# Optimization experiments

Hardware: AMD Instinct MI355X
Metric: run time of the kernel (lower is better)

The kernel has to match this reference:

```python
import jax, jax.numpy as jnp
import numpy as np

B, NV, FD = 16, 128, 8192
T_TEMP = 0.2      # self.T
MARGIN = 1.0      # nn.TripletMarginLoss default
EPS = 1e-6        # pairwise_distance eps


def _l2norm(x):
    # torch F.normalize(dim=1): x / max(||x||, 1e-12)
    nrm = jnp.maximum(jnp.linalg.norm(x, axis=-1, keepdims=True), 1e-12)
    return x / nrm


def _ssl_parts(qb, kb, nb, num_gt):
    # qb,kb,nb: [NV, FD] flattened reid embeddings for one image
    qv = _l2norm(qb)[:num_gt]          # [g, FD]
    kv = _l2norm(kb)[:num_gt]          # [g, FD]
    nv = _l2norm(nb)                   # [NV, FD] (negatives are NOT sliced)
    g = num_gt
    S = qv @ kv.T                      # [g, g] all pairwise dots (replaces torch.dot loops)
    # similarity-matrix loss
    sm = jnp.sum((S - jnp.eye(g, dtype=S.dtype)) ** 2) / (g * g)
    # pairwise distances with torch eps convention: ||a - b + eps||_2
    # = sqrt(||a||^2 + ||b||^2 - 2 a.b + 2*eps*(sum(a)-sum(b)) + D*eps^2); ||a||=||b||=1
    sq = qv.sum(axis=1)                # [g]
    sk = kv.sum(axis=1)                # [g]
    const = FD * EPS * EPS
    d_qk = jnp.sqrt(jnp.maximum(2.0 - 2.0 * S + 2.0 * EPS * (sq[:, None] - sk[None, :]) + const, 0.0))
    d_kq = jnp.sqrt(jnp.maximum(2.0 - 2.0 * S.T + 2.0 * EPS * (sk[:, None] - sq[None, :]) + const, 0.0))
    off = 1.0 - jnp.eye(g, dtype=S.dtype)
    # triplet: anc=q_i,pos=k_i,neg=k_j  and  anc=k_i,pos=q_i,neg=q_j, j != i
    tri1 = jnp.sum(jax.nn.relu(jnp.diag(d_qk)[:, None] - d_qk + MARGIN) * off)
    tri2 = jnp.sum(jax.nn.relu(jnp.diag(d_kq)[:, None] - d_kq + MARGIN) * off)
    tri_sum = tri1 + tri2
    # cycle consistency: |q_i.k_j - k_i.q_j| = |S[i,j] - S[j,i]|
    cyc = jnp.sum(jnp.abs(S - S.T) * off) / (g * (g - 1))
    # InfoNCE: l_pos = q_i.k_i, l_neg = q @ n.T
    l_pos = jnp.diag(S)[:, None]       # [g, 1]
    l_neg = qv @ nv.T                  # [g, NV]
    logits = jnp.concatenate([l_pos, l_neg], axis=1) / T_TEMP
    ce = jnp.mean(jax.nn.logsumexp(logits, axis=1) - logits[:, 0])  # CE with labels=0
    return sm, tri_sum, cyc, ce / g


def setup_inputs() -> dict:
    key = jax.random.key(0)
    kq, kk, kn = jax.random.split(key, 3)
    q = jax.random.normal(kq, (B, NV, FD), dtype=jnp.float32)
    k = jax.random.normal(kk, (B, NV, FD), dtype=jnp.float32)
    n = jax.random.normal(kn, (B, NV, FD), dtype=jnp.float32)
    return {"q": q, "k": k, "n": n, "num_gt": NV}


def reference(q, k, n, num_gt):
    sm, tri, cyc, ce = jax.vmap(lambda a, b, c: _ssl_parts(a, b, c, num_gt))(q, k, n)
    tri_cnt = 2 * num_gt * (num_gt - 1)
    # original bug: tri_loss accumulates across batches while tri_cnt resets,
    # so each batch contributes cumsum(tri)[b] / tri_cnt
    ssl = jnp.sum(sm) + jnp.sum(jnp.cumsum(tri)) / tri_cnt + jnp.sum(cyc) + jnp.sum(ce)
    return ssl
```

## Files before the change

kernel.cpp:

```cpp
#include <hip/hip_runtime.h>
#include <cstdint>
#include <cstddef>

#define B_N   16
#define G_N   128
#define FD_N  8192
#define KSPLIT 16
#define KC    512
#define BK2   32
#define NITER 16

typedef unsigned short u16;
typedef u16  u16x8 __attribute__((ext_vector_type(8)));
typedef __bf16 bf16x8 __attribute__((ext_vector_type(8)));
typedef float f32x16 __attribute__((ext_vector_type(16)));

#define QSUM_P   0
#define QSSQ_P   32768
#define KSUM_P   65536
#define KSSQ_P   98304
#define NSSQ_P   131072
#define SM_ROW   163840
#define CE_ROW   165888
#define S_OFF    167936
#define PART_OFF_F 430080

__device__ __forceinline__ u16 f2bf(float f) {
    uint32_t u = __float_as_uint(f);
    u += 0x7FFFu + ((u >> 16) & 1u);
    return (u16)(u >> 16);
}

__device__ __forceinline__ void load_lds16(const float* g, float* l) {
    __builtin_amdgcn_global_load_lds(
        (__attribute__((address_space(1))) void*)(g),
        (__attribute__((address_space(3))) void*)(l),
        16, 0, 0);
}

#define WAITV4() asm volatile("s_waitcnt vmcnt(4)" ::: "memory")
#define WAITV0() asm volatile("s_waitcnt vmcnt(0)" ::: "memory")

__global__ __launch_bounds__(512, 4)
void k_gemm(const float* __restrict__ q, const float* __restrict__ kM,
            const float* __restrict__ nM, float* __restrict__ ws)
{
    __shared__ __align__(16) float sA[2][G_N * BK2];
    __shared__ __align__(16) float sB[2][G_N * BK2];

    const int tid = threadIdx.x;
    const int blk = blockIdx.x;
    const int b    = blk >> 5;
    const int rem  = blk & 31;
    const int half = rem >> 4;
    const int kch  = rem & 15;

    const int lane  = tid & 63;
    const int wv    = tid >> 6;
    const int wm    = wv >> 2;
    const int wn    = wv & 3;
    const int khalf = lane >> 5;
    const int lrow  = lane & 31;
    const int rA0 = wm*64 + lrow;
    const int rB0 = wn*32 + lrow;
    const bool statA = (wn == 0);
    const bool statB = (wm == 0);

    const size_t mat_off = (size_t)b * (G_N * FD_N) + (size_t)kch * KC;
    const float* Ap = q + mat_off;
    const float* Bp = (half ? nM : kM) + mat_off;

    const int r0s = wv*16 + (lane >> 3);
    const int r1s = r0s + 8;
    const size_t goff0 = (size_t)r0s * FD_N + (size_t)(((lane & 7) ^ (r0s & 7)) << 2);
    const size_t goff1 = (size_t)r1s * FD_N + (size_t)(((lane & 7) ^ (r1s & 7)) << 2);
    const int lds0 = wv * 512;
    const int lds1 = wv * 512 + 256;

#define STAGE(ST, T) do {                                                     \
        const size_t tof_ = (size_t)((T) * BK2);                              \
        load_lds16(Ap + goff0 + tof_, &sA[ST][lds0]);                         \
        load_lds16(Bp + goff0 + tof_, &sB[ST][lds0]);                         \
        load_lds16(Ap + goff1 + tof_, &sA[ST][lds1]);                         \
        load_lds16(Bp + goff1 + tof_, &sB[ST][lds1]);                         \
    } while (0)

#define LOADCVT(SP, R, CH, FR, EN, SS, QQ) do {                               \
        const int x_ = (R) & 7;                                               \
        const float* rp_ = (SP) + (R) * BK2;                                  \
        float4 lo_ = *(const float4*)(rp_ + ((((CH)*2    ) ^ x_) << 2));      \
        float4 hi_ = *(const float4*)(rp_ + ((((CH)*2 + 1) ^ x_) << 2));      \
        if (EN) {                                                             \
            SS += (lo_.x + lo_.y) + (lo_.z + lo_.w)                           \
                + (hi_.x + hi_.y) + (hi_.z + hi_.w);                          \
            QQ += lo_.x*lo_.x + lo_.y*lo_.y + lo_.z*lo_.z + lo_.w*lo_.w       \
                + hi_.x*hi_.x + hi_.y*hi_.y + hi_.z*hi_.z + hi_.w*hi_.w;      \
        }                                                                     \
        u16x8 h_;                                                             \
        h_[0]=f2bf(lo_.x); h_[1]=f2bf(lo_.y); h_[2]=f2bf(lo_.z); h_[3]=f2bf(lo_.w); \
        h_[4]=f2bf(hi_.x); h_[5]=f2bf(hi_.y); h_[6]=f2bf(hi_.z); h_[7]=f2bf(hi_.w); \
        FR = __builtin_bit_cast(bf16x8, h_);                                  \
    } while (0)

#define COMPUTE_PHASE(ST) do {                                                \
        const float* sAp_ = &sA[ST][0];                                       \
        const float* sBp_ = &sB[ST][0];                                       \
        _Pragma("unroll")                                                     \
        for (int s = 0; s < 2; ++s) {                                         \
            const int ch = s*2 + khalf;                                       \
            bf16x8 af0, af1, bfv;                                             \
            LOADCVT(sAp_, rA0,      ch, af0, statA, aS0, aQ0);                \
            LOADCVT(sAp_, rA0 + 32, ch, af1, statA, aS1, aQ1);                \
            LOADCVT(sBp_, rB0,      ch, bfv, statB, bS0, bQ0);                \
            acc[0] = __builtin_amdgcn_mfma_f32_32x32x16_bf16(af0, bfv, acc[0], 0, 0, 0); \
            acc[1] = __builtin_amdgcn_mfma_f32_32x32x16_bf16(af1, bfv, acc[1], 0, 0, 0); \
        }                                                                     \
    } while (0)

    float aS0 = 0.f, aQ0 = 0.f, aS1 = 0.f, aQ1 = 0.f, bS0 = 0.f, bQ0 = 0.f;

    f32x16 acc[2];
    #pragma unroll
    for (int mb = 0; mb < 2; ++mb)
      #pragma unroll
      for (int e = 0; e < 16; ++e) acc[mb][e] = 0.f;

    STAGE(0, 0);
    STAGE(1, 1);

    for (int t = 0; t < 14; t += 2) {
        WAITV4();
        __builtin_amdgcn_s_barrier();
        COMPUTE_PHASE(0);
        __builtin_amdgcn_s_barrier();
        STAGE(0, t + 2);

        WAITV4();
        __builtin_amdgcn_s_barrier();
        COMPUTE_PHASE(1);
        __builtin_amdgcn_s_barrier();
        STAGE(1, t + 3);
    }
    WAITV4();
    __builtin_amdgcn_s_barrier();
    COMPUTE_PHASE(0);
    __builtin_amdgcn_s_barrier();
    WAITV0();
    __builtin_amdgcn_s_barrier();
    COMPUTE_PHASE(1);

    u16* part = (u16*)(ws + PART_OFF_F) + ((size_t)blk << 14);
    #pragma unroll
    for (int mb = 0; mb < 2; ++mb) {
        int col = wn*32 + lrow;
        int rbase = wm*64 + mb*32 + 4*khalf;
        #pragma unroll
        for (int reg = 0; reg < 16; ++reg) {
            int row = rbase + (reg & 3) + 8*(reg >> 2);
            part[row*G_N + col] = f2bf(acc[mb][reg]);
        }
    }

    if (statA) {
        aS0 += __shfl_xor(aS0, 32, 64); aQ0 += __shfl_xor(aQ0, 32, 64);
        aS1 += __shfl_xor(aS1, 32, 64); aQ1 += __shfl_xor(aQ1, 32, 64);
        if (half == 0 && khalf == 0) {
            int o = kch*2048 + b*G_N + wm*64 + lrow;
            ws[QSUM_P + o]      = aS0; ws[QSSQ_P + o]      = aQ0;
            ws[QSUM_P + o + 32] = aS1; ws[QSSQ_P + o + 32] = aQ1;
        }
    }
    if (statB) {
        bS0 += __shfl_xor(bS0, 32, 64); bQ0 += __shfl_xor(bQ0, 32, 64);
        if (khalf == 0) {
            int o = kch*2048 + b*G_N + wn*32 + lrow;
            if (half == 0) { ws[KSUM_P + o] = bS0; ws[KSSQ_P + o] = bQ0; }
            else           { ws[NSSQ_P + o] = bQ0; }
        }
    }
#undef STAGE
#undef LOADCVT
#undef COMPUTE_PHASE
}

__global__ __launch_bounds__(256)
void k_red2(float* __restrict__ ws, float* __restrict__ out)
{
    const int blk  = blockIdx.x;
    const int b    = blk >> 4;
    const int half = (blk >> 3) & 1;
    const int rg   = blk & 7;
    const int t    = threadIdx.x;
    const int lr   = t >> 4;
    const int i    = rg*16 + lr;
    const int c8   = t & 15;
    __shared__ float nrm[128];
    __shared__ float invq_s[16];

    if (blk == 0 && t == 0) out[0] = 0.f;

    if (t < 128) {
        float ss = 0.f;
        const float* p = ws + (half ? NSSQ_P : KSSQ_P) + b*G_N + t;
        #pragma unroll
        for (int kc2 = 0; kc2 < KSPLIT; ++kc2) ss += p[kc2*2048];
        nrm[t] = 1.f / fmaxf(sqrtf(ss), 1e-12f);
    } else if (t < 144) {
        float ss = 0.f;
        const float* p = ws + QSSQ_P + b*G_N + rg*16 + (t - 128);
        #pragma unroll
        for (int kc2 = 0; kc2 < KSPLIT; ++kc2) ss += p[kc2*2048];
        invq_s[t-128] = 1.f / fmaxf(sqrtf(ss), 1e-12f);
    }
    __syncthreads();

    const u16* part = (const u16*)(ws + PART_OFF_F);
    float s[8] = {0,0,0,0,0,0,0,0};
    #pragma unroll
    for (int kc2 = 0; kc2 < KSPLIT; ++kc2) {
        size_t idx = ((size_t)(b*32 + half*16 + kc2) << 14) + i*G_N + c8*8;
        u16x8 h = *(const u16x8*)(part + idx);
        #pragma unroll
        for (int e = 0; e < 8; ++e)
            s[e] += __uint_as_float(((uint32_t)h[e]) << 16);
    }
    const float iq = invq_s[lr];
    if (half == 0) {
        float smacc = 0.f;
        float S8[8];
        #pragma unroll
        for (int e = 0; e < 8; ++e) {
            int j = c8*8 + e;
            S8[e] = s[e] * iq * nrm[j];
            float d = S8[e] - (j == i ? 1.f : 0.f);
            smacc += d*d;
        }
        float* Sp = ws + S_OFF + (size_t)b*16384 + i*G_N + c8*8;
        float4 w0 = {S8[0],S8[1],S8[2],S8[3]};
        float4 w1 = {S8[4],S8[5],S8[6],S8[7]};
        *(float4*)Sp = w0; *(float4*)(Sp+4) = w1;
        #pragma unroll
        for (int m = 8; m >= 1; m >>= 1) smacc += __shfl_xor(smacc, m, 64);
        if (c8 == 0) ws[SM_ROW + b*G_N + i] = smacc;
    } else {
        float eacc = 0.f;
        #pragma unroll
        for (int e = 0; e < 8; ++e)
            eacc += __expf(5.f * s[e] * iq * nrm[c8*8+e]);
        #pragma unroll
        for (int m = 8; m >= 1; m >>= 1) eacc += __shfl_xor(eacc, m, 64);
        if (c8 == 0) ws[CE_ROW + b*G_N + i] = eacc;
    }
}

__global__ __launch_bounds__(256)
void k_epi(float* __restrict__ ws, float* __restrict__ out)
{
    const int blk = blockIdx.x;
    const int b   = blk >> 3;
    const int i0  = (blk & 7) * 16;
    const int t   = threadIdx.x;
    __shared__ float sqv[128], skv[128], ddq[128], ddk[128];
    __shared__ float rbuf[4];
    const float c0 = (float)FD_N * 1e-6f * 1e-6f;

    const float* S = ws + S_OFF + (size_t)b * 16384;
    if (t < 128) {
        float qs=0, qq=0, ks=0, kq=0;
        #pragma unroll
        for (int kc2 = 0; kc2 < KSPLIT; ++kc2) {
            int o = kc2*2048 + b*G_N + t;
            qs += ws[QSUM_P + o]; qq += ws[QSSQ_P + o];
            ks += ws[KSUM_P + o]; kq += ws[KSSQ_P + o];
        }
        float iq = 1.f/fmaxf(sqrtf(qq),1e-12f);
        float ik = 1.f/fmaxf(sqrtf(kq),1e-12f);
        float sq = qs*iq, sk = ks*ik;
        sqv[t]=sq; skv[t]=sk;
        float Stt = S[t*G_N + t];
        ddq[t] = sqrtf(fmaxf(2.f - 2.f*Stt + 2e-6f*(sq-sk) + c0, 0.f));
        ddk[t] = sqrtf(fmaxf(2.f - 2.f*Stt + 2e-6f*(sk-sq) + c0, 0.f));
    }
    __syncthreads();

    float tri=0.f, cyc=0.f, ce=0.f, sm=0.f;
    #pragma unroll
    for (int p = 0; p < 8; ++p) {
        int idx = p*256 + t;
        int i = i0 + (idx >> 7), j = idx & 127;
        if (i != j) {
            float S_ij = S[i*G_N + j];
            float dqk = sqrtf(fmaxf(2.f - 2.f*S_ij + 2e-6f*(sqv[i]-skv[j]) + c0, 0.f));
            tri += fmaxf(ddq[i] - dqk + 1.f, 0.f);
            float dkq = sqrtf(fmaxf(2.f - 2.f*S_ij + 2e-6f*(skv[j]-sqv[i]) + c0, 0.f));
            tri += fmaxf(ddk[j] - dkq + 1.f, 0.f);
            cyc += fabsf(S_ij - S[j*G_N + i]);
        }
    }
    if (t < 16) {
        int r = i0 + t;
        float lp = 5.f * S[r*G_N + r];
        ce = __logf(ws[CE_ROW + b*G_N + r] + __expf(lp)) - lp;
        sm = ws[SM_ROW + b*G_N + r];
    }
    float contrib = sm * (1.f/16384.f) + cyc * (1.f/16256.f) + ce * (1.f/16384.f)
                  + (float)(B_N - b) * tri * (1.f/32512.f);
    #pragma unroll
    for (int m = 32; m >= 1; m >>= 1) contrib += __shfl_xor(contrib, m, 64);
    if ((t & 63) == 0) rbuf[t >> 6] = contrib;
    __syncthreads();
    if (t == 0) atomicAdd(out, rbuf[0] + rbuf[1] + rbuf[2] + rbuf[3]);
}

extern "C" void kernel_launch(void* const* d_in, const int* in_sizes, int n_in,
                              void* d_out, int out_size, void* d_ws, size_t ws_size,
                              hipStream_t stream)
{
    const float* q  = (const float*)d_in[0];
    const float* kM = (const float*)d_in[1];
    const float* nM = (const float*)d_in[2];
    float* ws  = (float*)d_ws;
    float* out = (float*)d_out;

    k_gemm<<<B_N * 2 * KSPLIT, 512, 0, stream>>>(q, kM, nM, ws);
    k_red2<<<256, 256, 0, stream>>>(ws, out);
    k_epi<<<128, 256, 0, stream>>>(ws, out);
}
```

Baseline: 219.6 us.

## Restructure GEMM to stage q rows in LDS as bf16 and stream k/n from global

Each block now converts a 32-row by 2048-wide slice of q to bf16 once and keeps it in LDS (about 128 KB). Eight waves then stream k or n rows directly from global memory into MFMA operands, with no LDS double-buffering for B. The K split drops from 16 to 4 chunks, which shrinks the partial-sum buffer, changes its layout, and makes the reduction kernels cheaper. In exchange, k and n are re-read once per row group (four times in total, possibly absorbed by L2), only one block fits per CU, and global load latency is hidden only by loop unrolling.

```diff
diff --git a/kernel.cpp b/kernel.cpp
--- a/kernel.cpp
+++ b/kernel.cpp
@@ -5,10 +5,9 @@
 #define B_N   16
 #define G_N   128
 #define FD_N  8192
-#define KSPLIT 16
-#define KC    512
-#define BK2   32
-#define NITER 16
+#define KRED  4
+#define KCF   2048
+#define RG_N  4
 
 typedef unsigned short u16;
 typedef u16  u16x8 __attribute__((ext_vector_type(8)));
@@ -31,156 +30,97 @@
     return (u16)(u >> 16);
 }
 
-__device__ __forceinline__ void load_lds16(const float* g, float* l) {
-    __builtin_amdgcn_global_load_lds(
-        (__attribute__((address_space(1))) void*)(g),
-        (__attribute__((address_space(3))) void*)(l),
-        16, 0, 0);
-}
-
-#define WAITV4() asm volatile("s_waitcnt vmcnt(4)" ::: "memory")
-#define WAITV0() asm volatile("s_waitcnt vmcnt(0)" ::: "memory")
-
-__global__ __launch_bounds__(512, 4)
+__global__ __launch_bounds__(512, 2)
 void k_gemm(const float* __restrict__ q, const float* __restrict__ kM,
             const float* __restrict__ nM, float* __restrict__ ws)
 {
-    __shared__ __align__(16) float sA[2][G_N * BK2];
-    __shared__ __align__(16) float sB[2][G_N * BK2];
+    __shared__ __align__(16) u16 sA[32 * 2048];
 
     const int tid = threadIdx.x;
     const int blk = blockIdx.x;
-    const int b    = blk >> 5;
-    const int rem  = blk & 31;
-    const int half = rem >> 4;
-    const int kch  = rem & 15;
+    const int b   = blk >> 4;
+    const int rg  = (blk >> 2) & 3;
+    const int kch = blk & 3;
+
+    {
+        const int r = tid >> 4;
+        const int c = tid & 15;
+        const float* Arow = q + (size_t)(b*G_N + rg*32 + r) * FD_N + kch*KCF;
+        u16* aldrow = sA + r * 2048;
+        float ssA = 0.f, qqA = 0.f;
+        #pragma unroll
+        for (int j = 0; j < 16; ++j) {
+            const float4 lo = *(const float4*)(Arow + j*128 + c*8);
+            const float4 hi = *(const float4*)(Arow + j*128 + c*8 + 4);
+            ssA += (lo.x + lo.y) + (lo.z + lo.w) + (hi.x + hi.y) + (hi.z + hi.w);
+            qqA += lo.x*lo.x + lo.y*lo.y + lo.z*lo.z + lo.w*lo.w
+                 + hi.x*hi.x + hi.y*hi.y + hi.z*hi.z + hi.w*hi.w;
+            u16x8 h;
+            h[0]=f2bf(lo.x); h[1]=f2bf(lo.y); h[2]=f2bf(lo.z); h[3]=f2bf(lo.w);
+            h[4]=f2bf(hi.x); h[5]=f2bf(hi.y); h[6]=f2bf(hi.z); h[7]=f2bf(hi.w);
+            *(u16x8*)(aldrow + (((j*16 + c) ^ (r & 7)) << 3)) = h;
+        }
+        #pragma unroll
+        for (int m = 8; m >= 1; m >>= 1) {
+            ssA += __shfl_xor(ssA, m, 64);
+            qqA += __shfl_xor(qqA, m, 64);
+        }
+        if (c == 0) {
+            const int o = kch*2048 + b*G_N + rg*32 + r;
+            ws[QSUM_P + o] = ssA; ws[QSSQ_P + o] = qqA;
+        }
+    }
+    __syncthreads();
 
     const int lane  = tid & 63;
     const int wv    = tid >> 6;
-    const int wm    = wv >> 2;
-    const int wn    = wv & 3;
+    const int ho    = wv >> 2;
+    const int bcol  = (wv & 3) * 32;
+    const int lrow  = lane & 31;
     const int khalf = lane >> 5;
-    const int lrow  = lane & 31;
-    const int rA0 = wm*64 + lrow;
-    const int rB0 = wn*32 + lrow;
-    const bool statA = (wn == 0);
-    const bool statB = (wm == 0);
-
-    const size_t mat_off = (size_t)b * (G_N * FD_N) + (size_t)kch * KC;
-    const float* Ap = q + mat_off;
-    const float* Bp = (half ? nM : kM) + mat_off;
-
-    const int r0s = wv*16 + (lane >> 3);
-    const int r1s = r0s + 8;
-    const size_t goff0 = (size_t)r0s * FD_N + (size_t)(((lane & 7) ^ (r0s & 7)) << 2);
-    const size_t goff1 = (size_t)r1s * FD_N + (size_t)(((lane & 7) ^ (r1s & 7)) << 2);
-    const int lds0 = wv * 512;
-    const int lds1 = wv * 512 + 256;
-
-#define STAGE(ST, T) do {                                                     \
-        const size_t tof_ = (size_t)((T) * BK2);                              \
-        load_lds16(Ap + goff0 + tof_, &sA[ST][lds0]);                         \
-        load_lds16(Bp + goff0 + tof_, &sB[ST][lds0]);                         \
-        load_lds16(Ap + goff1 + tof_, &sA[ST][lds1]);                         \
-        load_lds16(Bp + goff1 + tof_, &sB[ST][lds1]);                         \
-    } while (0)
-
-#define LOADCVT(SP, R, CH, FR, EN, SS, QQ) do {                               \
-        const int x_ = (R) & 7;                                               \
-        const float* rp_ = (SP) + (R) * BK2;                                  \
-        float4 lo_ = *(const float4*)(rp_ + ((((CH)*2    ) ^ x_) << 2));      \
-        float4 hi_ = *(const float4*)(rp_ + ((((CH)*2 + 1) ^ x_) << 2));      \
-        if (EN) {                                                             \
-            SS += (lo_.x + lo_.y) + (lo_.z + lo_.w)                           \
-                + (hi_.x + hi_.y) + (hi_.z + hi_.w);                          \
-            QQ += lo_.x*lo_.x + lo_.y*lo_.y + lo_.z*lo_.z + lo_.w*lo_.w       \
-                + hi_.x*hi_.x + hi_.y*hi_.y + hi_.z*hi_.z + hi_.w*hi_.w;      \
-        }                                                                     \
-        u16x8 h_;                                                             \
-        h_[0]=f2bf(lo_.x); h_[1]=f2bf(lo_.y); h_[2]=f2bf(lo_.z); h_[3]=f2bf(lo_.w); \
-        h_[4]=f2bf(hi_.x); h_[5]=f2bf(hi_.y); h_[6]=f2bf(hi_.z); h_[7]=f2bf(hi_.w); \
-        FR = __builtin_bit_cast(bf16x8, h_);                                  \
-    } while (0)
-
-#define COMPUTE_PHASE(ST) do {                                                \
-        const float* sAp_ = &sA[ST][0];                                       \
-        const float* sBp_ = &sB[ST][0];                                       \
-        _Pragma("unroll")                                                     \
-        for (int s = 0; s < 2; ++s) {                                         \
-            const int ch = s*2 + khalf;                                       \
-            bf16x8 af0, af1, bfv;                                             \
-            LOADCVT(sAp_, rA0,      ch, af0, statA, aS0, aQ0);                \
-            LOADCVT(sAp_, rA0 + 32, ch, af1, statA, aS1, aQ1);                \
-            LOADCVT(sBp_, rB0,      ch, bfv, statB, bS0, bQ0);                \
-            acc[0] = __builtin_amdgcn_mfma_f32_32x32x16_bf16(af0, bfv, acc[0], 0, 0, 0); \
-            acc[1] = __builtin_amdgcn_mfma_f32_32x32x16_bf16(af1, bfv, acc[1], 0, 0, 0); \
-        }                                                                     \
-    } while (0)
-
-    float aS0 = 0.f, aQ0 = 0.f, aS1 = 0.f, aQ1 = 0.f, bS0 = 0.f, bQ0 = 0.f;
-
-    f32x16 acc[2];
-    #pragma unroll
-    for (int mb = 0; mb < 2; ++mb)
-      #pragma unroll
-      for (int e = 0; e < 16; ++e) acc[mb][e] = 0.f;
-
-    STAGE(0, 0);
-    STAGE(1, 1);
-
-    for (int t = 0; t < 14; t += 2) {
-        WAITV4();
-        __builtin_amdgcn_s_barrier();
-        COMPUTE_PHASE(0);
-        __builtin_amdgcn_s_barrier();
-        STAGE(0, t + 2);
-
-        WAITV4();
-        __builtin_amdgcn_s_barrier();
-        COMPUTE_PHASE(1);
-        __builtin_amdgcn_s_barrier();
-        STAGE(1, t + 3);
-    }
-    WAITV4();
-    __builtin_amdgcn_s_barrier();
-    COMPUTE_PHASE(0);
-    __builtin_amdgcn_s_barrier();
-    WAITV0();
-    __builtin_amdgcn_s_barrier();
-    COMPUTE_PHASE(1);
-
-    u16* part = (u16*)(ws + PART_OFF_F) + ((size_t)blk << 14);
-    #pragma unroll
-    for (int mb = 0; mb < 2; ++mb) {
-        int col = wn*32 + lrow;
-        int rbase = wm*64 + mb*32 + 4*khalf;
+
+    const float* Brow = (ho ? nM : kM)
+        + (size_t)(b*G_N + bcol + lrow) * FD_N + kch*KCF + khalf*8;
+    const u16* afr = sA + lrow * 2048;
+
+    f32x16 acc;
+    #pragma unroll
+    for (int e = 0; e < 16; ++e) acc[e] = 0.f;
+    float ssB = 0.f, qqB = 0.f;
+
+    #pragma unroll 8
+    for (int kc = 0; kc < 128; ++kc) {
+        const float4 lo = *(const float4*)(Brow + kc*16);
+        const float4 hi = *(const float4*)(Brow + kc*16 + 4);
+        ssB += (lo.x + lo.y) + (lo.z + lo.w) + (hi.x + hi.y) + (hi.z + hi.w);
+        qqB += lo.x*lo.x + lo.y*lo.y + lo.z*lo.z + lo.w*lo.w
+             + hi.x*hi.x + hi.y*hi.y + hi.z*hi.z + hi.w*hi.w;
+        u16x8 hb;
+        hb[0]=f2bf(lo.x); hb[1]=f2bf(lo.y); hb[2]=f2bf(lo.z); hb[3]=f2bf(lo.w);
+        hb[4]=f2bf(hi.x); hb[5]=f2bf(hi.y); hb[6]=f2bf(hi.z); hb[7]=f2bf(hi.w);
+        const bf16x8 bfv = __builtin_bit_cast(bf16x8, hb);
+        const bf16x8 afv = __builtin_bit_cast(bf16x8,
+            *(const u16x8*)(afr + ((((kc*2 + khalf) ^ (lrow & 7))) << 3)));
+        acc = __builtin_amdgcn_mfma_f32_32x32x16_bf16(afv, bfv, acc, 0, 0, 0);
+    }
+
+    {
+        u16* pb = (u16*)(ws + PART_OFF_F) + (size_t)(b*2 + ho) * 65536;
+        const int col = bcol + lrow;
         #pragma unroll
         for (int reg = 0; reg < 16; ++reg) {
-            int row = rbase + (reg & 3) + 8*(reg >> 2);
-            part[row*G_N + col] = f2bf(acc[mb][reg]);
-        }
-    }
-
-    if (statA) {
-        aS0 += __shfl_xor(aS0, 32, 64); aQ0 += __shfl_xor(aQ0, 32, 64);
-        aS1 += __shfl_xor(aS1, 32, 64); aQ1 += __shfl_xor(aQ1, 32, 64);
-        if (half == 0 && khalf == 0) {
-            int o = kch*2048 + b*G_N + wm*64 + lrow;
-            ws[QSUM_P + o]      = aS0; ws[QSSQ_P + o]      = aQ0;
-            ws[QSUM_P + o + 32] = aS1; ws[QSSQ_P + o + 32] = aQ1;
-        }
-    }
-    if (statB) {
-        bS0 += __shfl_xor(bS0, 32, 64); bQ0 += __shfl_xor(bQ0, 32, 64);
-        if (khalf == 0) {
-            int o = kch*2048 + b*G_N + wn*32 + lrow;
-            if (half == 0) { ws[KSUM_P + o] = bS0; ws[KSSQ_P + o] = bQ0; }
-            else           { ws[NSSQ_P + o] = bQ0; }
-        }
-    }
-#undef STAGE
-#undef LOADCVT
-#undef COMPUTE_PHASE
+            const int row = rg*32 + (reg & 3) + 8*(reg >> 2) + 4*khalf;
+            pb[(row*4 + kch)*128 + col] = f2bf(acc[reg]);
+        }
+    }
+
+    ssB += __shfl_xor(ssB, 32, 64);
+    qqB += __shfl_xor(qqB, 32, 64);
+    if (rg == 0 && khalf == 0) {
+        const int o = kch*2048 + b*G_N + bcol + lrow;
+        if (ho == 0) { ws[KSUM_P + o] = ssB; ws[KSSQ_P + o] = qqB; }
+        else         { ws[NSSQ_P + o] = qqB; }
+    }
 }
 
 __global__ __launch_bounds__(256)
@@ -203,23 +143,22 @@
         float ss = 0.f;
         const float* p = ws + (half ? NSSQ_P : KSSQ_P) + b*G_N + t;
         #pragma unroll
-        for (int kc2 = 0; kc2 < KSPLIT; ++kc2) ss += p[kc2*2048];
+        for (int kc2 = 0; kc2 < KRED; ++kc2) ss += p[kc2*2048];
         nrm[t] = 1.f / fmaxf(sqrtf(ss), 1e-12f);
     } else if (t < 144) {
         float ss = 0.f;
         const float* p = ws + QSSQ_P + b*G_N + rg*16 + (t - 128);
         #pragma unroll
-        for (int kc2 = 0; kc2 < KSPLIT; ++kc2) ss += p[kc2*2048];
+        for (int kc2 = 0; kc2 < KRED; ++kc2) ss += p[kc2*2048];
         invq_s[t-128] = 1.f / fmaxf(sqrtf(ss), 1e-12f);
     }
     __syncthreads();
 
-    const u16* part = (const u16*)(ws + PART_OFF_F);
+    const u16* part = (const u16*)(ws + PART_OFF_F) + (size_t)(b*2 + half) * 65536;
     float s[8] = {0,0,0,0,0,0,0,0};
     #pragma unroll
-    for (int kc2 = 0; kc2 < KSPLIT; ++kc2) {
-        size_t idx = ((size_t)(b*32 + half*16 + kc2) << 14) + i*G_N + c8*8;
-        u16x8 h = *(const u16x8*)(part + idx);
+    for (int kc2 = 0; kc2 < KRED; ++kc2) {
+        u16x8 h = *(const u16x8*)(part + (size_t)(i*4 + kc2)*128 + c8*8);
         #pragma unroll
         for (int e = 0; e < 8; ++e)
             s[e] += __uint_as_float(((uint32_t)h[e]) << 16);
@@ -268,7 +207,7 @@
     if (t < 128) {
         float qs=0, qq=0, ks=0, kq=0;
         #pragma unroll
-        for (int kc2 = 0; kc2 < KSPLIT; ++kc2) {
+        for (int kc2 = 0; kc2 < KRED; ++kc2) {
             int o = kc2*2048 + b*G_N + t;
             qs += ws[QSUM_P + o]; qq += ws[QSSQ_P + o];
             ks += ws[KSUM_P + o]; kq += ws[KSSQ_P + o];
@@ -322,7 +261,7 @@
     float* ws  = (float*)d_ws;
     float* out = (float*)d_out;
 
-    k_gemm<<<B_N * 2 * KSPLIT, 512, 0, stream>>>(q, kM, nM, ws);
+    k_gemm<<<B_N * RG_N * KRED, 512, 0, stream>>>(q, kM, nM, ws);
     k_red2<<<256, 256, 0, stream>>>(ws, out);
     k_epi<<<128, 256, 0, stream>>>(ws, out);
 }
```

New measurement: 272.6 us. 1.24x slower.

## Split fp32-to-bf16 conversion and row stats into a prep kernel before the GEMM

Applied to the files above, without the earlier changes.

Adds a prep kernel that reads each fp32 row of q, k and n once, writes a bf16 copy to workspace, and computes each row's sum and sum of squares in full. The GEMM kernel then stages bf16 tiles straight into LDS with wider K-steps, fewer K-chunks (8 instead of 16) and raised wave priority around the MFMAs, removing the in-loop conversion and stats work. The reduction kernels read the single per-row stats instead of summing 16 partials. The trade-off is an extra launch and an extra write and read of the bf16 copy (about half the fp32 input size) through global memory, and the GEMM grid shrinks from 512 to 256 blocks.

```diff
diff --git a/kernel.cpp b/kernel.cpp
--- a/kernel.cpp
+++ b/kernel.cpp
@@ -5,12 +5,14 @@
 #define B_N   16
 #define G_N   128
 #define FD_N  8192
-#define KSPLIT 16
-#define KC    512
-#define BK2   32
-#define NITER 16
+#define KCH_N 8
+#define KCB   1024
+#define BKB   64
+#define NST   16
+#define NROWS 6144
 
 typedef unsigned short u16;
+typedef u16  u16x4 __attribute__((ext_vector_type(4)));
 typedef u16  u16x8 __attribute__((ext_vector_type(8)));
 typedef __bf16 bf16x8 __attribute__((ext_vector_type(8)));
 typedef float f32x16 __attribute__((ext_vector_type(16)));
@@ -24,6 +26,7 @@
 #define CE_ROW   165888
 #define S_OFF    167936
 #define PART_OFF_F 430080
+#define BF16_OFF_F 2527232
 
 __device__ __forceinline__ u16 f2bf(float f) {
     uint32_t u = __float_as_uint(f);
@@ -41,19 +44,53 @@
 #define WAITV4() asm volatile("s_waitcnt vmcnt(4)" ::: "memory")
 #define WAITV0() asm volatile("s_waitcnt vmcnt(0)" ::: "memory")
 
-__global__ __launch_bounds__(512, 4)
-void k_gemm(const float* __restrict__ q, const float* __restrict__ kM,
+__global__ __launch_bounds__(256)
+void k_prep(const float* __restrict__ q, const float* __restrict__ kM,
             const float* __restrict__ nM, float* __restrict__ ws)
 {
-    __shared__ __align__(16) float sA[2][G_N * BK2];
-    __shared__ __align__(16) float sB[2][G_N * BK2];
+    const int lane = threadIdx.x & 63;
+    const int wv   = threadIdx.x >> 6;
+    const int R    = blockIdx.x * 4 + wv;
+    const int mat  = R >> 11;
+    const int r    = R & 2047;
+
+    const float* src = (mat == 0 ? q : (mat == 1 ? kM : nM)) + (size_t)r * FD_N;
+    u16* dst = (u16*)(ws + BF16_OFF_F) + (size_t)R * FD_N;
+
+    float ss = 0.f, qq = 0.f;
+    #pragma unroll 8
+    for (int j = 0; j < 32; ++j) {
+        const float4 v = *(const float4*)(src + (size_t)(j*64 + lane)*4);
+        ss += (v.x + v.y) + (v.z + v.w);
+        qq += v.x*v.x + v.y*v.y + v.z*v.z + v.w*v.w;
+        u16x4 h;
+        h[0]=f2bf(v.x); h[1]=f2bf(v.y); h[2]=f2bf(v.z); h[3]=f2bf(v.w);
+        *(u16x4*)(dst + (size_t)(j*64 + lane)*4) = h;
+    }
+    #pragma unroll
+    for (int m = 32; m >= 1; m >>= 1) {
+        ss += __shfl_xor(ss, m, 64);
+        qq += __shfl_xor(qq, m, 64);
+    }
+    if (lane == 0) {
+        if (mat == 0)      { ws[QSUM_P + r] = ss; ws[QSSQ_P + r] = qq; }
+        else if (mat == 1) { ws[KSUM_P + r] = ss; ws[KSSQ_P + r] = qq; }
+        else               { ws[NSSQ_P + r] = qq; }
+    }
+}
+
+__global__ __launch_bounds__(512, 2)
+void k_mm(float* __restrict__ ws)
+{
+    __shared__ __align__(16) u16 sA[2][G_N * BKB];
+    __shared__ __align__(16) u16 sB[2][G_N * BKB];
 
     const int tid = threadIdx.x;
     const int blk = blockIdx.x;
-    const int b    = blk >> 5;
-    const int rem  = blk & 31;
-    const int half = rem >> 4;
-    const int kch  = rem & 15;
+    const int b    = blk >> 4;
+    const int rem  = blk & 15;
+    const int half = rem >> 3;
+    const int kch  = rem & 7;
 
     const int lane  = tid & 63;
     const int wv    = tid >> 6;
@@ -63,61 +100,42 @@
     const int lrow  = lane & 31;
     const int rA0 = wm*64 + lrow;
     const int rB0 = wn*32 + lrow;
-    const bool statA = (wn == 0);
-    const bool statB = (wm == 0);
-
-    const size_t mat_off = (size_t)b * (G_N * FD_N) + (size_t)kch * KC;
-    const float* Ap = q + mat_off;
-    const float* Bp = (half ? nM : kM) + mat_off;
-
-    const int r0s = wv*16 + (lane >> 3);
-    const int r1s = r0s + 8;
-    const size_t goff0 = (size_t)r0s * FD_N + (size_t)(((lane & 7) ^ (r0s & 7)) << 2);
-    const size_t goff1 = (size_t)r1s * FD_N + (size_t)(((lane & 7) ^ (r1s & 7)) << 2);
-    const int lds0 = wv * 512;
-    const int lds1 = wv * 512 + 256;
+
+    const u16* bf = (const u16*)(ws + BF16_OFF_F);
+    const u16* Abase = bf + (size_t)(b*G_N) * FD_N + kch*KCB;
+    const u16* Bbase = bf + (size_t)(((half ? 2 : 1)*2048) + b*G_N) * FD_N + kch*KCB;
+
+    const int srow = wv*16 + (lane >> 3);
+    const size_t gsw = (size_t)srow * FD_N + (size_t)(((lane & 7) ^ (srow & 7)) << 3);
+    const int l0 = wv * 1024;
+    const int l1 = l0 + 512;
 
 #define STAGE(ST, T) do {                                                     \
-        const size_t tof_ = (size_t)((T) * BK2);                              \
-        load_lds16(Ap + goff0 + tof_, &sA[ST][lds0]);                         \
-        load_lds16(Bp + goff0 + tof_, &sB[ST][lds0]);                         \
-        load_lds16(Ap + goff1 + tof_, &sA[ST][lds1]);                         \
-        load_lds16(Bp + goff1 + tof_, &sB[ST][lds1]);                         \
+        const size_t tof_ = gsw + (size_t)((T) * BKB);                        \
+        load_lds16((const float*)(Abase + tof_),            (float*)(&sA[ST][l0])); \
+        load_lds16((const float*)(Bbase + tof_),            (float*)(&sB[ST][l0])); \
+        load_lds16((const float*)(Abase + tof_ + 8*FD_N),   (float*)(&sA[ST][l1])); \
+        load_lds16((const float*)(Bbase + tof_ + 8*FD_N),   (float*)(&sB[ST][l1])); \
     } while (0)
 
-#define LOADCVT(SP, R, CH, FR, EN, SS, QQ) do {                               \
-        const int x_ = (R) & 7;                                               \
-        const float* rp_ = (SP) + (R) * BK2;                                  \
-        float4 lo_ = *(const float4*)(rp_ + ((((CH)*2    ) ^ x_) << 2));      \
-        float4 hi_ = *(const float4*)(rp_ + ((((CH)*2 + 1) ^ x_) << 2));      \
-        if (EN) {                                                             \
-            SS += (lo_.x + lo_.y) + (lo_.z + lo_.w)                           \
-                + (hi_.x + hi_.y) + (hi_.z + hi_.w);                          \
-            QQ += lo_.x*lo_.x + lo_.y*lo_.y + lo_.z*lo_.z + lo_.w*lo_.w       \
-                + hi_.x*hi_.x + hi_.y*hi_.y + hi_.z*hi_.z + hi_.w*hi_.w;      \
+#define FRAG(SP, R, KC)                                                       \
+    __builtin_bit_cast(bf16x8, *(const u16x8*)((SP) + (R)*BKB +               \
+        ((((KC)*2 + khalf) ^ ((R)&7)) << 3)))
+
+#define COMPUTE(ST) do {                                                      \
+        const u16* dA_ = &sA[ST][0];                                          \
+        const u16* dB_ = &sB[ST][0];                                          \
+        __builtin_amdgcn_s_setprio(1);                                        \
+        _Pragma("unroll")                                                     \
+        for (int kc = 0; kc < 4; ++kc) {                                      \
+            bf16x8 a0_ = FRAG(dA_, rA0,      kc);                             \
+            bf16x8 a1_ = FRAG(dA_, rA0 + 32, kc);                             \
+            bf16x8 b0_ = FRAG(dB_, rB0,      kc);                             \
+            acc[0] = __builtin_amdgcn_mfma_f32_32x32x16_bf16(a0_, b0_, acc[0], 0,0,0); \
+            acc[1] = __builtin_amdgcn_mfma_f32_32x32x16_bf16(a1_, b0_, acc[1], 0,0,0); \
         }                                                                     \
-        u16x8 h_;                                                             \
-        h_[0]=f2bf(lo_.x); h_[1]=f2bf(lo_.y); h_[2]=f2bf(lo_.z); h_[3]=f2bf(lo_.w); \
-        h_[4]=f2bf(hi_.x); h_[5]=f2bf(hi_.y); h_[6]=f2bf(hi_.z); h_[7]=f2bf(hi_.w); \
-        FR = __builtin_bit_cast(bf16x8, h_);                                  \
+        __builtin_amdgcn_s_setprio(0);                                        \
     } while (0)
-
-#define COMPUTE_PHASE(ST) do {                                                \
-        const float* sAp_ = &sA[ST][0];                                       \
-        const float* sBp_ = &sB[ST][0];                                       \
-        _Pragma("unroll")                                                     \
-        for (int s = 0; s < 2; ++s) {                                         \
-            const int ch = s*2 + khalf;                                       \
-            bf16x8 af0, af1, bfv;                                             \
-            LOADCVT(sAp_, rA0,      ch, af0, statA, aS0, aQ0);                \
-            LOADCVT(sAp_, rA0 + 32, ch, af1, statA, aS1, aQ1);                \
-            LOADCVT(sBp_, rB0,      ch, bfv, statB, bS0, bQ0);                \
-            acc[0] = __builtin_amdgcn_mfma_f32_32x32x16_bf16(af0, bfv, acc[0], 0, 0, 0); \
-            acc[1] = __builtin_amdgcn_mfma_f32_32x32x16_bf16(af1, bfv, acc[1], 0, 0, 0); \
-        }                                                                     \
-    } while (0)
-
-    float aS0 = 0.f, aQ0 = 0.f, aS1 = 0.f, aQ1 = 0.f, bS0 = 0.f, bQ0 = 0.f;
 
     f32x16 acc[2];
     #pragma unroll
@@ -128,59 +146,41 @@
     STAGE(0, 0);
     STAGE(1, 1);
 
-    for (int t = 0; t < 14; t += 2) {
+    for (int t = 0; t < NST - 2; t += 2) {
         WAITV4();
         __builtin_amdgcn_s_barrier();
-        COMPUTE_PHASE(0);
+        COMPUTE(0);
         __builtin_amdgcn_s_barrier();
         STAGE(0, t + 2);
 
         WAITV4();
         __builtin_amdgcn_s_barrier();
-        COMPUTE_PHASE(1);
+        COMPUTE(1);
         __builtin_amdgcn_s_barrier();
         STAGE(1, t + 3);
     }
     WAITV4();
     __builtin_amdgcn_s_barrier();
-    COMPUTE_PHASE(0);
+    COMPUTE(0);
     __builtin_amdgcn_s_barrier();
     WAITV0();
     __builtin_amdgcn_s_barrier();
-    COMPUTE_PHASE(1);
+    COMPUTE(1);
 
     u16* part = (u16*)(ws + PART_OFF_F) + ((size_t)blk << 14);
     #pragma unroll
     for (int mb = 0; mb < 2; ++mb) {
-        int col = wn*32 + lrow;
-        int rbase = wm*64 + mb*32 + 4*khalf;
+        const int col = wn*32 + lrow;
+        const int rbase = wm*64 + mb*32 + 4*khalf;
         #pragma unroll
         for (int reg = 0; reg < 16; ++reg) {
-            int row = rbase + (reg & 3) + 8*(reg >> 2);
+            const int row = rbase + (reg & 3) + 8*(reg >> 2);
             part[row*G_N + col] = f2bf(acc[mb][reg]);
         }
     }
-
-    if (statA) {
-        aS0 += __shfl_xor(aS0, 32, 64); aQ0 += __shfl_xor(aQ0, 32, 64);
-        aS1 += __shfl_xor(aS1, 32, 64); aQ1 += __shfl_xor(aQ1, 32, 64);
-        if (half == 0 && khalf == 0) {
-            int o = kch*2048 + b*G_N + wm*64 + lrow;
-            ws[QSUM_P + o]      = aS0; ws[QSSQ_P + o]      = aQ0;
-            ws[QSUM_P + o + 32] = aS1; ws[QSSQ_P + o + 32] = aQ1;
-        }
-    }
-    if (statB) {
-        bS0 += __shfl_xor(bS0, 32, 64); bQ0 += __shfl_xor(bQ0, 32, 64);
-        if (khalf == 0) {
-            int o = kch*2048 + b*G_N + wn*32 + lrow;
-            if (half == 0) { ws[KSUM_P + o] = bS0; ws[KSSQ_P + o] = bQ0; }
-            else           { ws[NSSQ_P + o] = bQ0; }
-        }
-    }
 #undef STAGE
-#undef LOADCVT
-#undef COMPUTE_PHASE
+#undef FRAG
+#undef COMPUTE
 }
 
 __global__ __launch_bounds__(256)
@@ -200,16 +200,10 @@
     if (blk == 0 && t == 0) out[0] = 0.f;
 
     if (t < 128) {
-        float ss = 0.f;
-        const float* p = ws + (half ? NSSQ_P : KSSQ_P) + b*G_N + t;
-        #pragma unroll
-        for (int kc2 = 0; kc2 < KSPLIT; ++kc2) ss += p[kc2*2048];
+        const float ss = ws[(half ? NSSQ_P : KSSQ_P) + b*G_N + t];
         nrm[t] = 1.f / fmaxf(sqrtf(ss), 1e-12f);
     } else if (t < 144) {
-        float ss = 0.f;
-        const float* p = ws + QSSQ_P + b*G_N + rg*16 + (t - 128);
-        #pragma unroll
-        for (int kc2 = 0; kc2 < KSPLIT; ++kc2) ss += p[kc2*2048];
+        const float ss = ws[QSSQ_P + b*G_N + rg*16 + (t - 128)];
         invq_s[t-128] = 1.f / fmaxf(sqrtf(ss), 1e-12f);
     }
     __syncthreads();
@@ -217,8 +211,8 @@
     const u16* part = (const u16*)(ws + PART_OFF_F);
     float s[8] = {0,0,0,0,0,0,0,0};
     #pragma unroll
-    for (int kc2 = 0; kc2 < KSPLIT; ++kc2) {
-        size_t idx = ((size_t)(b*32 + half*16 + kc2) << 14) + i*G_N + c8*8;
+    for (int kc2 = 0; kc2 < KCH_N; ++kc2) {
+        const size_t idx = ((size_t)(b*16 + half*8 + kc2) << 14) + i*G_N + c8*8;
         u16x8 h = *(const u16x8*)(part + idx);
         #pragma unroll
         for (int e = 0; e < 8; ++e)
@@ -266,13 +260,10 @@
 
     const float* S = ws + S_OFF + (size_t)b * 16384;
     if (t < 128) {
-        float qs=0, qq=0, ks=0, kq=0;
-        #pragma unroll
-        for (int kc2 = 0; kc2 < KSPLIT; ++kc2) {
-            int o = kc2*2048 + b*G_N + t;
-            qs += ws[QSUM_P + o]; qq += ws[QSSQ_P + o];
-            ks += ws[KSUM_P + o]; kq += ws[KSSQ_P + o];
-        }
+        const float qs = ws[QSUM_P + b*G_N + t];
+        const float qq = ws[QSSQ_P + b*G_N + t];
+        const float ks = ws[KSUM_P + b*G_N + t];
+        const float kq = ws[KSSQ_P + b*G_N + t];
         float iq = 1.f/fmaxf(sqrtf(qq),1e-12f);
         float ik = 1.f/fmaxf(sqrtf(kq),1e-12f);
         float sq = qs*iq, sk = ks*ik;
@@ -322,7 +313,8 @@
     float* ws  = (float*)d_ws;
     float* out = (float*)d_out;
 
-    k_gemm<<<B_N * 2 * KSPLIT, 512, 0, stream>>>(q, kM, nM, ws);
+    k_prep<<<NROWS/4, 256, 0, stream>>>(q, kM, nM, ws);
+    k_mm<<<256, 512, 0, stream>>>(ws);
     k_red2<<<256, 256, 0, stream>>>(ws, out);
     k_epi<<<128, 256, 0, stream>>>(ws, out);
 }
```

New measurement: 252.9 us. +15.1%, slower.
